# Optimization experiments

Hardware: AMD Instinct MI355X
Metric: run time of the kernel (lower is better)

The kernel has to match this reference:

```python
import jax, jax.numpy as jnp
import numpy as np

C_RED = 8
BN_EPS = 1e-5
NORM_EPS = 1e-6

# pairwise upper-triangular index lists (static, matches torch buffers)
_idx_i, _idx_j = [], []
for _i in range(C_RED):
    for _j in range(_i, C_RED):
        _idx_i.append(_i)
        _idx_j.append(_j)
IDX_I = np.array(_idx_i, dtype=np.int32)
IDX_J = np.array(_idx_j, dtype=np.int32)


def setup_inputs() -> dict:
    key = jax.random.key(0)
    ks = jax.random.split(key, 8)
    B, Cin, H, W = 32, 256, 56, 56
    x = jax.random.normal(ks[0], (B, Cin, H, W), dtype=jnp.float32)
    w_reduce = jax.random.normal(ks[1], (C_RED, Cin, 1, 1), dtype=jnp.float32) * 0.05
    bn_gamma = jax.random.uniform(ks[2], (C_RED,), dtype=jnp.float32, minval=0.5, maxval=1.5)
    bn_beta = jax.random.normal(ks[3], (C_RED,), dtype=jnp.float32) * 0.1
    bn_mean = jax.random.normal(ks[4], (C_RED,), dtype=jnp.float32) * 0.1
    bn_var = jax.random.uniform(ks[5], (C_RED,), dtype=jnp.float32, minval=0.5, maxval=1.5)
    w_dw = jax.random.normal(ks[6], (C_RED, 1, 3, 3), dtype=jnp.float32) * 0.3
    scale = jax.random.uniform(ks[7], (1, C_RED, 1, 1), dtype=jnp.float32, minval=0.5, maxval=1.5)
    return {"x": x, "w_reduce": w_reduce, "bn_gamma": bn_gamma, "bn_beta": bn_beta,
            "bn_mean": bn_mean, "bn_var": bn_var, "w_dw": w_dw, "scale": scale}


def _l2norm_ch(z):
    # F.normalize(p=2, dim=1, eps=1e-6): x / max(||x||_2, eps)
    n = jnp.sqrt(jnp.sum(z * z, axis=1, keepdims=True))
    return z / jnp.maximum(n, NORM_EPS)


def reference(x, w_reduce, bn_gamma, bn_beta, bn_mean, bn_var, w_dw, scale):
    # 1x1 conv (no bias)
    z = jax.lax.conv_general_dilated(x, w_reduce, (1, 1), 'VALID',
                                     dimension_numbers=('NCHW', 'OIHW', 'NCHW'))
    # BatchNorm (inference) + ReLU
    inv = bn_gamma / jnp.sqrt(bn_var + BN_EPS)
    z = z * inv[None, :, None, None] + (bn_beta - bn_mean * inv)[None, :, None, None]
    z = jax.nn.relu(z)
    # depthwise 3x3 twist conv, padding 1, times per-channel scale
    z_twist = jax.lax.conv_general_dilated(z, w_dw, (1, 1), ((1, 1), (1, 1)),
                                           dimension_numbers=('NCHW', 'OIHW', 'NCHW'),
                                           feature_group_count=C_RED) * scale
    z_norm = _l2norm_ch(z)
    z_twist_norm = _l2norm_ch(z_twist)
    # gathered pairwise products over upper-triangular channel pairs
    interactions = jnp.take(z_norm, IDX_I, axis=1) * jnp.take(z_twist_norm, IDX_J, axis=1)
    return jnp.concatenate([z_norm, interactions], axis=1)  # [B, 8+36, H, W]
```

## Files before the change

kernel.cpp:

```cpp
#include <hip/hip_runtime.h>

#define BATCH 32
#define CIN   256
#define CR    8
#define HDIM  56
#define WDIM  56
#define HW    3136
#define COUT  44

__global__ __launch_bounds__(64) void k1_reduce_bn_relu(
    const float* __restrict__ x, const float* __restrict__ wr,
    const float* __restrict__ gamma, const float* __restrict__ beta,
    const float* __restrict__ mean, const float* __restrict__ var,
    float* __restrict__ z)
{
    const int t = blockIdx.x * 64 + threadIdx.x;
    const int b = t / HW;
    const int p = t - b * HW;
    const float* xp = x + (size_t)b * CIN * HW + p;

    float acc[CR];
#pragma unroll
    for (int c = 0; c < CR; ++c) acc[c] = 0.f;

#pragma unroll 16
    for (int cin = 0; cin < CIN; ++cin) {
        const float xv = xp[(size_t)cin * HW];
#pragma unroll
        for (int c = 0; c < CR; ++c)
            acc[c] = fmaf(xv, wr[c * CIN + cin], acc[c]);
    }

    float v[CR];
#pragma unroll
    for (int c = 0; c < CR; ++c) {
        const float inv = gamma[c] / sqrtf(var[c] + 1e-5f);
        const float sh  = beta[c] - mean[c] * inv;
        v[c] = fmaxf(fmaf(acc[c], inv, sh), 0.f);
    }

    float4* zp = reinterpret_cast<float4*>(z + (size_t)t * CR);
    zp[0] = make_float4(v[0], v[1], v[2], v[3]);
    zp[1] = make_float4(v[4], v[5], v[6], v[7]);
}

__global__ __launch_bounds__(64) void k2_dw_norm_inter(
    const float* __restrict__ z, const float* __restrict__ wdw,
    const float* __restrict__ scale, float* __restrict__ out)
{
    const int t = blockIdx.x * 64 + threadIdx.x;
    const int b = t / HW;
    const int p = t - b * HW;
    const int h = p / WDIM;
    const int w = p - h * WDIM;

    const float4 c0 = reinterpret_cast<const float4*>(z + (size_t)t * CR)[0];
    const float4 c1 = reinterpret_cast<const float4*>(z + (size_t)t * CR)[1];
    const float zc[CR] = {c0.x, c0.y, c0.z, c0.w, c1.x, c1.y, c1.z, c1.w};

    float tw[CR];
#pragma unroll
    for (int c = 0; c < CR; ++c) tw[c] = 0.f;

#pragma unroll
    for (int dy = -1; dy <= 1; ++dy) {
        const int hh = h + dy;
        const bool okh = (hh >= 0) && (hh < HDIM);
#pragma unroll
        for (int dx = -1; dx <= 1; ++dx) {
            const int ww = w + dx;
            const bool ok = okh && (ww >= 0) && (ww < WDIM);
            if (ok) {
                const float* zn = z + ((size_t)(b * HW + hh * WDIM + ww)) * CR;
                const float4 n0 = reinterpret_cast<const float4*>(zn)[0];
                const float4 n1 = reinterpret_cast<const float4*>(zn)[1];
                const float nv[CR] = {n0.x, n0.y, n0.z, n0.w, n1.x, n1.y, n1.z, n1.w};
                const int k = (dy + 1) * 3 + (dx + 1);
#pragma unroll
                for (int c = 0; c < CR; ++c)
                    tw[c] = fmaf(nv[c], wdw[c * 9 + k], tw[c]);
            }
        }
    }

    float s1 = 0.f, s2 = 0.f;
#pragma unroll
    for (int c = 0; c < CR; ++c) {
        tw[c] *= scale[c];
        s1 = fmaf(zc[c], zc[c], s1);
        s2 = fmaf(tw[c], tw[c], s2);
    }
    const float r1 = 1.0f / fmaxf(sqrtf(s1), 1e-6f);
    const float r2 = 1.0f / fmaxf(sqrtf(s2), 1e-6f);

    float a[CR], tb[CR];
#pragma unroll
    for (int c = 0; c < CR; ++c) { a[c] = zc[c] * r1; tb[c] = tw[c] * r2; }

    float* op = out + (size_t)b * COUT * HW + p;
#pragma unroll
    for (int c = 0; c < CR; ++c)
        op[(size_t)c * HW] = a[c];

    int idx = CR;
#pragma unroll
    for (int i = 0; i < CR; ++i) {
#pragma unroll
        for (int j = i; j < CR; ++j) {
            op[(size_t)idx * HW] = a[i] * tb[j];
            ++idx;
        }
    }
}

extern "C" void kernel_launch(void* const* d_in, const int* in_sizes, int n_in,
                              void* d_out, int out_size, void* d_ws, size_t ws_size,
                              hipStream_t stream) {
    const float* x     = (const float*)d_in[0];
    const float* wr    = (const float*)d_in[1];
    const float* gamma = (const float*)d_in[2];
    const float* beta  = (const float*)d_in[3];
    const float* mean  = (const float*)d_in[4];
    const float* var   = (const float*)d_in[5];
    const float* wdw   = (const float*)d_in[6];
    const float* scale = (const float*)d_in[7];
    float* out = (float*)d_out;
    float* z   = (float*)d_ws;

    const int npix = BATCH * HW;
    k1_reduce_bn_relu<<<npix / 64, 64, 0, stream>>>(x, wr, gamma, beta, mean, var, z);
    k2_dw_norm_inter<<<npix / 64, 64, 0, stream>>>(z, wdw, scale, out);
}
```

Before: 181.8 us.

## Split channel reduction across four waves per block and branchless depthwise stencil

The 1x1 reduce kernel now gives each 64-pixel tile to four waves, each summing a quarter of the input channels. The partial sums are combined through shared memory, and the final z write is coalesced across pixel×channel. This adds memory-level parallelism for the dominant x read, with 16 loads batched per step, at the cost of a block barrier and LDS traffic. The depthwise kernel uses 256-thread blocks, reuses the centre value, and replaces the boundary branches with clamped loads plus a mask multiply to avoid divergence.

```diff
diff --git a/kernel.cpp b/kernel.cpp
--- a/kernel.cpp
+++ b/kernel.cpp
@@ -8,47 +8,67 @@
 #define HW    3136
 #define COUT  44
 
-__global__ __launch_bounds__(64) void k1_reduce_bn_relu(
+__global__ __launch_bounds__(256) void k1_reduce_bn_relu(
     const float* __restrict__ x, const float* __restrict__ wr,
     const float* __restrict__ gamma, const float* __restrict__ beta,
     const float* __restrict__ mean, const float* __restrict__ var,
     float* __restrict__ z)
 {
-    const int t = blockIdx.x * 64 + threadIdx.x;
-    const int b = t / HW;
-    const int p = t - b * HW;
-    const float* xp = x + (size_t)b * CIN * HW + p;
+    const int lane = threadIdx.x & 63;
+    const int wv   = __builtin_amdgcn_readfirstlane(threadIdx.x >> 6);
+    const int pix0 = blockIdx.x * 64;
+    const int gp   = pix0 + lane;
+    const int b    = gp / HW;
+    const int p    = gp - b * HW;
+    const int cin0 = wv * 64;
+
+    const float* __restrict__ xq =
+        x + (size_t)b * CIN * HW + (size_t)cin0 * HW + p;
 
     float acc[CR];
 #pragma unroll
     for (int c = 0; c < CR; ++c) acc[c] = 0.f;
 
-#pragma unroll 16
-    for (int cin = 0; cin < CIN; ++cin) {
-        const float xv = xp[(size_t)cin * HW];
+    for (int k0 = 0; k0 < 64; k0 += 16) {
+        float xv[16];
 #pragma unroll
-        for (int c = 0; c < CR; ++c)
-            acc[c] = fmaf(xv, wr[c * CIN + cin], acc[c]);
+        for (int j = 0; j < 16; ++j)
+            xv[j] = xq[(size_t)(k0 + j) * HW];
+#pragma unroll
+        for (int j = 0; j < 16; ++j) {
+            const int cin = cin0 + k0 + j;
+#pragma unroll
+            for (int c = 0; c < CR; ++c)
+                acc[c] = fmaf(xv[j], wr[c * CIN + cin], acc[c]);
+        }
     }
 
-    float v[CR];
+    __shared__ float pacc[4][64][CR];
 #pragma unroll
-    for (int c = 0; c < CR; ++c) {
-        const float inv = gamma[c] / sqrtf(var[c] + 1e-5f);
-        const float sh  = beta[c] - mean[c] * inv;
-        v[c] = fmaxf(fmaf(acc[c], inv, sh), 0.f);
+    for (int c = 0; c < CR; c += 4)
+        *reinterpret_cast<float4*>(&pacc[wv][lane][c]) =
+            make_float4(acc[c], acc[c + 1], acc[c + 2], acc[c + 3]);
+    __syncthreads();
+
+    const int t = threadIdx.x;
+    const int c = t & 7;
+    const float inv = gamma[c] / sqrtf(var[c] + 1e-5f);
+    const float sh  = beta[c] - mean[c] * inv;
+    float* zb = z + (size_t)pix0 * CR;
+#pragma unroll
+    for (int e = t; e < 512; e += 256) {
+        const int px = e >> 3;
+        const float s = pacc[0][px][c] + pacc[1][px][c]
+                      + pacc[2][px][c] + pacc[3][px][c];
+        zb[e] = fmaxf(fmaf(s, inv, sh), 0.f);
     }
-
-    float4* zp = reinterpret_cast<float4*>(z + (size_t)t * CR);
-    zp[0] = make_float4(v[0], v[1], v[2], v[3]);
-    zp[1] = make_float4(v[4], v[5], v[6], v[7]);
 }
 
-__global__ __launch_bounds__(64) void k2_dw_norm_inter(
+__global__ __launch_bounds__(256) void k2_dw_norm_inter(
     const float* __restrict__ z, const float* __restrict__ wdw,
     const float* __restrict__ scale, float* __restrict__ out)
 {
-    const int t = blockIdx.x * 64 + threadIdx.x;
+    const int t = blockIdx.x * 256 + threadIdx.x;
     const int b = t / HW;
     const int p = t - b * HW;
     const int h = p / WDIM;
@@ -60,26 +80,27 @@
 
     float tw[CR];
 #pragma unroll
-    for (int c = 0; c < CR; ++c) tw[c] = 0.f;
+    for (int c = 0; c < CR; ++c) tw[c] = zc[c] * wdw[c * 9 + 4];
 
+    const float* __restrict__ zimg = z + (size_t)b * HW * CR;
 #pragma unroll
     for (int dy = -1; dy <= 1; ++dy) {
-        const int hh = h + dy;
-        const bool okh = (hh >= 0) && (hh < HDIM);
 #pragma unroll
         for (int dx = -1; dx <= 1; ++dx) {
-            const int ww = w + dx;
-            const bool ok = okh && (ww >= 0) && (ww < WDIM);
-            if (ok) {
-                const float* zn = z + ((size_t)(b * HW + hh * WDIM + ww)) * CR;
-                const float4 n0 = reinterpret_cast<const float4*>(zn)[0];
-                const float4 n1 = reinterpret_cast<const float4*>(zn)[1];
-                const float nv[CR] = {n0.x, n0.y, n0.z, n0.w, n1.x, n1.y, n1.z, n1.w};
-                const int k = (dy + 1) * 3 + (dx + 1);
+            if (dy == 0 && dx == 0) continue;
+            const int hh = h + dy, ww = w + dx;
+            const bool ok = (hh >= 0) & (hh < HDIM) & (ww >= 0) & (ww < WDIM);
+            const int hc = min(max(hh, 0), HDIM - 1);
+            const int wc = min(max(ww, 0), WDIM - 1);
+            const float m = ok ? 1.0f : 0.0f;
+            const float* zn = zimg + (size_t)(hc * WDIM + wc) * CR;
+            const float4 n0 = reinterpret_cast<const float4*>(zn)[0];
+            const float4 n1 = reinterpret_cast<const float4*>(zn)[1];
+            const float nv[CR] = {n0.x, n0.y, n0.z, n0.w, n1.x, n1.y, n1.z, n1.w};
+            const int k = (dy + 1) * 3 + (dx + 1);
 #pragma unroll
-                for (int c = 0; c < CR; ++c)
-                    tw[c] = fmaf(nv[c], wdw[c * 9 + k], tw[c]);
-            }
+            for (int c = 0; c < CR; ++c)
+                tw[c] = fmaf(nv[c] * m, wdw[c * 9 + k], tw[c]);
         }
     }
 
@@ -128,6 +149,6 @@
     float* z   = (float*)d_ws;
 
     const int npix = BATCH * HW;
-    k1_reduce_bn_relu<<<npix / 64, 64, 0, stream>>>(x, wr, gamma, beta, mean, var, z);
-    k2_dw_norm_inter<<<npix / 64, 64, 0, stream>>>(z, wdw, scale, out);
+    k1_reduce_bn_relu<<<npix / 64, 256, 0, stream>>>(x, wr, gamma, beta, mean, var, z);
+    k2_dw_norm_inter<<<npix / 256, 256, 0, stream>>>(z, wdw, scale, out);
 }
```

Measured after the change: 176.3 us. 3.0% less time.

## Fuse reduce conv and depthwise/interaction stages into one banded kernel with LDS halo

Applied to the files above, without the earlier changes.

Merges the two kernels into one. Each 512-thread block computes the 1x1 reduce, BN and ReLU for a 7-row band plus one halo row above and below, stages it in shared memory, then computes the depthwise conv, the normalisations and the pairwise outputs from LDS. This removes the global z round-trip and the second launch, and double-buffers the x loads across channels. In exchange, about 2/9 of the reduce work is recomputed for halo rows, and the grid shrinks to 256 large blocks, which lowers parallelism on a memory-bound read of x.

```diff
diff --git a/kernel.cpp b/kernel.cpp
--- a/kernel.cpp
+++ b/kernel.cpp
@@ -8,107 +8,135 @@
 #define HW    3136
 #define COUT  44
 
-__global__ __launch_bounds__(64) void k1_reduce_bn_relu(
+#define RB    7
+#define ZROWS 9
+#define ZPX   (ZROWS*WDIM)
+#define IPX   (RB*WDIM)
+#define LDSW  512
+
+__global__ __launch_bounds__(512) void fused_head(
     const float* __restrict__ x, const float* __restrict__ wr,
     const float* __restrict__ gamma, const float* __restrict__ beta,
     const float* __restrict__ mean, const float* __restrict__ var,
-    float* __restrict__ z)
+    const float* __restrict__ wdw, const float* __restrict__ scale,
+    float* __restrict__ out)
 {
-    const int t = blockIdx.x * 64 + threadIdx.x;
-    const int b = t / HW;
-    const int p = t - b * HW;
-    const float* xp = x + (size_t)b * CIN * HW + p;
+    __shared__ float zs[CR][LDSW];
 
-    float acc[CR];
+    const int blk  = blockIdx.x;
+    const int b    = blk & 31;
+    const int band = blk >> 5;
+    const int r0   = band * RB;
+    const int tid  = threadIdx.x;
+
+    {
+        const int px  = tid;
+        const int lr  = px / WDIM;
+        const int col = px - lr * WDIM;
+        const int gr  = r0 - 1 + lr;
+        const bool rowok = (gr >= 0) && (gr < HDIM);
+        const int grc = min(max(gr, 0), HDIM - 1);
+        const float* __restrict__ xp =
+            x + (size_t)b * CIN * HW + (size_t)grc * WDIM + col;
+
+        float acc[CR];
 #pragma unroll
-    for (int c = 0; c < CR; ++c) acc[c] = 0.f;
+        for (int c = 0; c < CR; ++c) acc[c] = 0.f;
 
-#pragma unroll 16
-    for (int cin = 0; cin < CIN; ++cin) {
-        const float xv = xp[(size_t)cin * HW];
+        float xa[16], xb[16];
+        auto loadx = [&](float (&arr)[16], int base) {
 #pragma unroll
-        for (int c = 0; c < CR; ++c)
-            acc[c] = fmaf(xv, wr[c * CIN + cin], acc[c]);
-    }
-
-    float v[CR];
+            for (int j = 0; j < 16; ++j)
+                arr[j] = xp[(size_t)(base + j) * HW];
+        };
+        auto consume = [&](const float (&arr)[16], int base) {
 #pragma unroll
-    for (int c = 0; c < CR; ++c) {
-        const float inv = gamma[c] / sqrtf(var[c] + 1e-5f);
-        const float sh  = beta[c] - mean[c] * inv;
-        v[c] = fmaxf(fmaf(acc[c], inv, sh), 0.f);
-    }
-
-    float4* zp = reinterpret_cast<float4*>(z + (size_t)t * CR);
-    zp[0] = make_float4(v[0], v[1], v[2], v[3]);
-    zp[1] = make_float4(v[4], v[5], v[6], v[7]);
-}
-
-__global__ __launch_bounds__(64) void k2_dw_norm_inter(
-    const float* __restrict__ z, const float* __restrict__ wdw,
-    const float* __restrict__ scale, float* __restrict__ out)
-{
-    const int t = blockIdx.x * 64 + threadIdx.x;
-    const int b = t / HW;
-    const int p = t - b * HW;
-    const int h = p / WDIM;
-    const int w = p - h * WDIM;
-
-    const float4 c0 = reinterpret_cast<const float4*>(z + (size_t)t * CR)[0];
-    const float4 c1 = reinterpret_cast<const float4*>(z + (size_t)t * CR)[1];
-    const float zc[CR] = {c0.x, c0.y, c0.z, c0.w, c1.x, c1.y, c1.z, c1.w};
-
-    float tw[CR];
-#pragma unroll
-    for (int c = 0; c < CR; ++c) tw[c] = 0.f;
-
-#pragma unroll
-    for (int dy = -1; dy <= 1; ++dy) {
-        const int hh = h + dy;
-        const bool okh = (hh >= 0) && (hh < HDIM);
-#pragma unroll
-        for (int dx = -1; dx <= 1; ++dx) {
-            const int ww = w + dx;
-            const bool ok = okh && (ww >= 0) && (ww < WDIM);
-            if (ok) {
-                const float* zn = z + ((size_t)(b * HW + hh * WDIM + ww)) * CR;
-                const float4 n0 = reinterpret_cast<const float4*>(zn)[0];
-                const float4 n1 = reinterpret_cast<const float4*>(zn)[1];
-                const float nv[CR] = {n0.x, n0.y, n0.z, n0.w, n1.x, n1.y, n1.z, n1.w};
-                const int k = (dy + 1) * 3 + (dx + 1);
+            for (int j = 0; j < 16; ++j) {
+                const int cin = base + j;
 #pragma unroll
                 for (int c = 0; c < CR; ++c)
-                    tw[c] = fmaf(nv[c], wdw[c * 9 + k], tw[c]);
+                    acc[c] = fmaf(arr[j], wr[c * CIN + cin], acc[c]);
+            }
+        };
+
+        loadx(xa, 0);
+        loadx(xb, 16);
+#pragma unroll
+        for (int k0 = 0; k0 < CIN; k0 += 32) {
+            consume(xa, k0);
+            if (k0 + 32 < CIN) loadx(xa, k0 + 32);
+            consume(xb, k0 + 16);
+            if (k0 + 48 < CIN) loadx(xb, k0 + 48);
+        }
+
+        if (px < ZPX) {
+#pragma unroll
+            for (int c = 0; c < CR; ++c) {
+                const float inv = gamma[c] / sqrtf(var[c] + 1e-5f);
+                const float sh  = beta[c] - mean[c] * inv;
+                const float v   = fmaxf(fmaf(acc[c], inv, sh), 0.f);
+                zs[c][px] = rowok ? v : 0.f;
             }
         }
     }
+    __syncthreads();
 
-    float s1 = 0.f, s2 = 0.f;
+    if (tid < IPX) {
+        const int p   = tid;
+        const int f   = p + WDIM;
+        const int lr  = p / WDIM;
+        const int col = p - lr * WDIM;
+
+        float zc[CR];
 #pragma unroll
-    for (int c = 0; c < CR; ++c) {
-        tw[c] *= scale[c];
-        s1 = fmaf(zc[c], zc[c], s1);
-        s2 = fmaf(tw[c], tw[c], s2);
-    }
-    const float r1 = 1.0f / fmaxf(sqrtf(s1), 1e-6f);
-    const float r2 = 1.0f / fmaxf(sqrtf(s2), 1e-6f);
+        for (int c = 0; c < CR; ++c) zc[c] = zs[c][f];
 
-    float a[CR], tb[CR];
+        float tw[CR];
 #pragma unroll
-    for (int c = 0; c < CR; ++c) { a[c] = zc[c] * r1; tb[c] = tw[c] * r2; }
+        for (int c = 0; c < CR; ++c) tw[c] = 0.f;
 
-    float* op = out + (size_t)b * COUT * HW + p;
 #pragma unroll
-    for (int c = 0; c < CR; ++c)
-        op[(size_t)c * HW] = a[c];
+        for (int dy = -1; dy <= 1; ++dy) {
+#pragma unroll
+            for (int dx = -1; dx <= 1; ++dx) {
+                const int k = (dy + 1) * 3 + (dx + 1);
+                const float m = (dx == 0) ? 1.f
+                              : (dx < 0 ? (col > 0  ? 1.f : 0.f)
+                                        : (col < WDIM - 1 ? 1.f : 0.f));
+                const int idx = max(f + dy * WDIM + dx, 0);
+#pragma unroll
+                for (int c = 0; c < CR; ++c)
+                    tw[c] = fmaf(zs[c][idx] * m, wdw[c * 9 + k], tw[c]);
+            }
+        }
 
-    int idx = CR;
+        float s1 = 0.f, s2 = 0.f;
 #pragma unroll
-    for (int i = 0; i < CR; ++i) {
+        for (int c = 0; c < CR; ++c) {
+            tw[c] *= scale[c];
+            s1 = fmaf(zc[c], zc[c], s1);
+            s2 = fmaf(tw[c], tw[c], s2);
+        }
+        const float r1 = 1.0f / fmaxf(sqrtf(s1), 1e-6f);
+        const float r2 = 1.0f / fmaxf(sqrtf(s2), 1e-6f);
+
+        float a[CR], tb[CR];
 #pragma unroll
-        for (int j = i; j < CR; ++j) {
-            op[(size_t)idx * HW] = a[i] * tb[j];
-            ++idx;
+        for (int c = 0; c < CR; ++c) { a[c] = zc[c] * r1; tb[c] = tw[c] * r2; }
+
+        float* op = out + (size_t)b * COUT * HW + (size_t)r0 * WDIM + p;
+#pragma unroll
+        for (int c = 0; c < CR; ++c)
+            op[(size_t)c * HW] = a[c];
+
+        int idx = CR;
+#pragma unroll
+        for (int i = 0; i < CR; ++i) {
+#pragma unroll
+            for (int j = i; j < CR; ++j) {
+                op[(size_t)idx * HW] = a[i] * tb[j];
+                ++idx;
+            }
         }
     }
 }
@@ -125,9 +153,8 @@
     const float* wdw   = (const float*)d_in[6];
     const float* scale = (const float*)d_in[7];
     float* out = (float*)d_out;
-    float* z   = (float*)d_ws;
+    (void)d_ws; (void)ws_size;
 
-    const int npix = BATCH * HW;
-    k1_reduce_bn_relu<<<npix / 64, 64, 0, stream>>>(x, wr, gamma, beta, mean, var, z);
-    k2_dw_norm_inter<<<npix / 64, 64, 0, stream>>>(z, wdw, scale, out);
+    fused_head<<<BATCH * 8, 512, 0, stream>>>(x, wr, gamma, beta, mean, var,
+                                              wdw, scale, out);
 }
```

Result: slower. 225.8 us (+24.2%).
